# Optimization experiments

Hardware: AMD Instinct MI355X
Metric: run time of the kernel (lower is better)

The kernel has to match this reference:

```python
import jax, jax.numpy as jnp
import numpy as np

N = 100000      # num_nodes
R = 8           # num_relations
D = 128         # node feature size
EMB = 128       # embedding_size
E = 1600000     # num edges
B = 16384       # batch of triples


def setup_inputs() -> dict:
    key = jax.random.key(0)
    ks = jax.random.split(key, 10)
    edge_src = jax.random.randint(ks[0], (E,), 0, N, dtype=jnp.int32)
    edge_dst = jax.random.randint(ks[1], (E,), 0, N, dtype=jnp.int32)
    edge_rel = jax.random.randint(ks[2], (E,), 0, R, dtype=jnp.int32)
    tri_nodes = jax.random.randint(ks[3], (B, 2), 0, N, dtype=jnp.int32)
    tri_rel = jax.random.randint(ks[4], (B,), 0, R, dtype=jnp.int32)
    X = jax.random.normal(ks[5], (N, D), dtype=jnp.float32)            # frozen node features
    W_rel = jax.random.normal(ks[6], (R, D, EMB), dtype=jnp.float32) * (1.0 / np.sqrt(D))
    W_self = jax.random.normal(ks[7], (D, EMB), dtype=jnp.float32) * (1.0 / np.sqrt(D))
    b = jnp.zeros((EMB,), dtype=jnp.float32)
    rel_emb = jax.random.normal(ks[8], (R, EMB), dtype=jnp.float32) * (1.0 / np.sqrt(EMB))  # xavier-ish
    return {"X": X, "W_rel": W_rel, "W_self": W_self, "b": b, "rel_emb": rel_emb,
            "edge_src": edge_src, "edge_dst": edge_dst, "edge_rel": edge_rel,
            "tri_nodes": tri_nodes, "tri_rel": tri_rel}


def _rgcn_layer(X, W_rel, W_self, b, edge_src, edge_dst, edge_rel):
    # per-relation transformed features: [R, N, EMB]
    XW = jnp.einsum('nd,rde->rne', X, W_rel)
    # gather per-edge messages: [E, EMB]
    msg = XW[edge_rel, edge_src]
    # RGCN normalization 1/c_{i,r}: count of (dst, rel) pairs
    comb = edge_dst.astype(jnp.int32) * R + edge_rel
    cnt = jax.ops.segment_sum(jnp.ones_like(comb, dtype=jnp.float32), comb, num_segments=N * R)
    norm = 1.0 / jnp.maximum(cnt[comb], 1.0)
    agg = jax.ops.segment_sum(msg * norm[:, None], edge_dst, num_segments=N)  # [N, EMB]
    return jax.nn.relu(agg + X @ W_self + b)


def reference(X, W_rel, W_self, b, rel_emb, edge_src, edge_dst, edge_rel, tri_nodes, tri_rel):
    H = _rgcn_layer(X, W_rel, W_self, b, edge_src, edge_dst, edge_rel)  # [N, EMB]
    subj = H[tri_nodes[:, 0]]          # [B, EMB]
    obj = H[tri_nodes[:, 1]]           # [B, EMB]
    rel = rel_emb[tri_rel]             # [B, EMB]
    scores = jnp.sum(subj * rel * obj, axis=1, keepdims=True)  # [B, 1]
    return scores
```

## Files before the change

### kernel.cpp

```cpp
#include <hip/hip_runtime.h>

typedef float f32x4 __attribute__((ext_vector_type(4)));
typedef short bf16x8 __attribute__((ext_vector_type(8)));

__device__ __forceinline__ unsigned short f2bf(float f) {
  unsigned int u = __float_as_uint(f);
  u += 0x7FFFu + ((u >> 16) & 1u);
  return (unsigned short)(u >> 16);
}

__global__ void k_build_map(const int* __restrict__ tri_nodes, int* __restrict__ map,
                            int* __restrict__ uniq, int* __restrict__ counter, int n) {
  int i = blockIdx.x * blockDim.x + threadIdx.x;
  if (i >= n) return;
  int node = tri_nodes[i];
  int old = atomicCAS(&map[node], -1, -2);
  if (old == -1) {
    int mid = atomicAdd(counter, 1);
    uniq[mid] = node;
    map[node] = mid;
  }
}

__global__ void k_count(const int* __restrict__ edst, const int* __restrict__ erel,
                        const int* __restrict__ map, int* __restrict__ cnt_c, int E) {
  int stride = gridDim.x * blockDim.x;
  for (int i = blockIdx.x * blockDim.x + threadIdx.x; i < E; i += stride) {
    int mid = map[edst[i]];
    if (mid >= 0) atomicAdd(&cnt_c[mid * 8 + erel[i]], 1);
  }
}

__global__ __launch_bounds__(256) void k_scan_s1(const int* __restrict__ cnt_c,
                                                 int* __restrict__ bsum) {
  __shared__ int sh[256];
  int tid = threadIdx.x;
  int base = blockIdx.x * 1024 + tid * 4;
  int s = cnt_c[base] + cnt_c[base + 1] + cnt_c[base + 2] + cnt_c[base + 3];
  sh[tid] = s;
  __syncthreads();
  for (int o = 1; o < 256; o <<= 1) {
    int x = (tid >= o) ? sh[tid - o] : 0;
    __syncthreads();
    sh[tid] += x;
    __syncthreads();
  }
  if (tid == 255) bsum[blockIdx.x] = sh[255];
}
__global__ __launch_bounds__(256) void k_scan_s2(int* __restrict__ bsum,
                                                 int* __restrict__ seg_start, int M) {
  __shared__ int sh[256];
  int tid = threadIdx.x;
  int v = bsum[tid];
  sh[tid] = v;
  __syncthreads();
  for (int o = 1; o < 256; o <<= 1) {
    int x = (tid >= o) ? sh[tid - o] : 0;
    __syncthreads();
    sh[tid] += x;
    __syncthreads();
  }
  bsum[tid] = sh[tid] - v;
  if (tid == 255) seg_start[M] = sh[255];
}
__global__ __launch_bounds__(256) void k_scan_s3(const int* __restrict__ cnt_c,
                                                 const int* __restrict__ bsum,
                                                 int* __restrict__ seg_start,
                                                 int* __restrict__ seg_ofs) {
  __shared__ int sh[256];
  int tid = threadIdx.x;
  int base = blockIdx.x * 1024 + tid * 4;
  int c0 = cnt_c[base], c1 = cnt_c[base + 1], c2 = cnt_c[base + 2], c3 = cnt_c[base + 3];
  int s = c0 + c1 + c2 + c3;
  sh[tid] = s;
  __syncthreads();
  for (int o = 1; o < 256; o <<= 1) {
    int x = (tid >= o) ? sh[tid - o] : 0;
    __syncthreads();
    sh[tid] += x;
    __syncthreads();
  }
  int run = bsum[blockIdx.x] + sh[tid] - s;
  seg_start[base] = run; seg_ofs[base] = run; run += c0;
  seg_start[base + 1] = run; seg_ofs[base + 1] = run; run += c1;
  seg_start[base + 2] = run; seg_ofs[base + 2] = run; run += c2;
  seg_start[base + 3] = run; seg_ofs[base + 3] = run;
}

__global__ void k_scatter(const int* __restrict__ esrc, const int* __restrict__ edst,
                          const int* __restrict__ erel, const int* __restrict__ map,
                          int* __restrict__ seg_ofs, int* __restrict__ s_src, int E) {
  int stride = gridDim.x * blockDim.x;
  for (int i = blockIdx.x * blockDim.x + threadIdx.x; i < E; i += stride) {
    int mid = map[edst[i]];
    if (mid >= 0) {
      int comb = mid * 8 + erel[i];
      int pos = atomicAdd(&seg_ofs[comb], 1);
      s_src[pos] = esrc[i];
    }
  }
}

__global__ void k_cvt_w(const float* __restrict__ W_rel, const float* __restrict__ W_self,
                        unsigned short* __restrict__ Wt) {
  int i = blockIdx.x * 256 + threadIdx.x;
  if (i >= 9 * 16384) return;
  int r = i >> 14, rem = i & 16383;
  int e = rem >> 7, d = rem & 127;
  float v = (r < 8) ? W_rel[r * 16384 + d * 128 + e] : W_self[d * 128 + e];
  Wt[i] = f2bf(v);
}

__global__ __launch_bounds__(512) void k_fused(
    const float* __restrict__ X, const unsigned short* __restrict__ Wt,
    const float* __restrict__ bvec, const int* __restrict__ uniq,
    const int* __restrict__ counter, const int* __restrict__ seg_start,
    const int* __restrict__ s_src, float* __restrict__ Hacc) {
  __shared__ __align__(16) unsigned short a_lds[64 * 128];
  __shared__ __align__(16) unsigned short w_lds[128 * 128];

  int nm = *counter;
  int mid0 = blockIdx.x * 64;
  if (mid0 >= nm) return;

  int t = threadIdx.x;
  int er = t >> 3, oct = t & 7;
  int lane = t & 63, l15 = lane & 15, lg = lane >> 4;
  int wid = t >> 6, wr = wid >> 2, wc = wid & 3;
  int mid = mid0 + er;

  f32x4 acc[2][2];
#pragma unroll
  for (int m = 0; m < 2; ++m)
#pragma unroll
    for (int n = 0; n < 2; ++n) {
      f32x4 z = {0.f, 0.f, 0.f, 0.f};
      acc[m][n] = z;
    }

  for (int r = 0; r < 9; ++r) {
    __syncthreads();

    {
      const uint4* wg = (const uint4*)(Wt + r * 16384);
#pragma unroll
      for (int i = 0; i < 4; ++i) {
        int v = t + i * 512;
        int u = v ^ ((v >> 4) & 7);
        *(uint4*)&w_lds[u * 8] = wg[v];
      }
    }

    {
      float aa[16];
#pragma unroll
      for (int q = 0; q < 16; ++q) aa[q] = 0.f;
      if (r < 8) {
        int comb = mid * 8 + r;
        int s0 = seg_start[comb], s1 = seg_start[comb + 1];
        for (int e = s0; e < s1; ++e) {
          const float4* xr = (const float4*)(X + (size_t)s_src[e] * 128) + oct * 4;
#pragma unroll
          for (int q = 0; q < 4; ++q) {
            float4 v = xr[q];
            aa[q * 4 + 0] += v.x; aa[q * 4 + 1] += v.y;
            aa[q * 4 + 2] += v.z; aa[q * 4 + 3] += v.w;
          }
        }
        int cnt = s1 - s0;
        if (cnt > 1) {
          float sc = 1.0f / (float)cnt;
#pragma unroll
          for (int q = 0; q < 16; ++q) aa[q] *= sc;
        }
      } else if (mid < nm) {
        const float4* xr = (const float4*)(X + (size_t)uniq[mid] * 128) + oct * 4;
#pragma unroll
        for (int q = 0; q < 4; ++q) {
          float4 v = xr[q];
          aa[q * 4 + 0] = v.x; aa[q * 4 + 1] = v.y;
          aa[q * 4 + 2] = v.z; aa[q * 4 + 3] = v.w;
        }
      }
      unsigned int p[8];
#pragma unroll
      for (int q = 0; q < 8; ++q)
        p[q] = (unsigned int)f2bf(aa[q * 2]) | ((unsigned int)f2bf(aa[q * 2 + 1]) << 16);
      int unit0 = er * 16 + oct * 2, sw = er & 7;
      uint4 p0 = make_uint4(p[0], p[1], p[2], p[3]);
      uint4 p1 = make_uint4(p[4], p[5], p[6], p[7]);
      *(uint4*)&a_lds[((unit0) ^ sw) * 8] = p0;
      *(uint4*)&a_lds[((unit0 + 1) ^ sw) * 8] = p1;
    }
    __syncthreads();

#pragma unroll
    for (int kb = 0; kb < 4; ++kb) {
      int ku = kb * 4 + lg;
      bf16x8 af[2], bfr[2];
#pragma unroll
      for (int m = 0; m < 2; ++m) {
        int row = wr * 32 + m * 16 + l15;
        af[m] = *(const bf16x8*)&a_lds[((row * 16 + ku) ^ (row & 7)) * 8];
      }
#pragma unroll
      for (int n = 0; n < 2; ++n) {
        int col = wc * 32 + n * 16 + l15;
        bfr[n] = *(const bf16x8*)&w_lds[((col * 16 + ku) ^ (col & 7)) * 8];
      }
#pragma unroll
      for (int m = 0; m < 2; ++m)
#pragma unroll
        for (int n = 0; n < 2; ++n)
          acc[m][n] = __builtin_amdgcn_mfma_f32_16x16x32_bf16(af[m], bfr[n], acc[m][n], 0, 0, 0);
    }
  }

#pragma unroll
  for (int m = 0; m < 2; ++m) {
#pragma unroll
    for (int n = 0; n < 2; ++n) {
      int col = wc * 32 + n * 16 + l15;
      float bv = bvec[col];
#pragma unroll
      for (int q = 0; q < 4; ++q) {
        int row = mid0 + wr * 32 + m * 16 + lg * 4 + q;
        float v = acc[m][n][q] + bv;
        Hacc[(size_t)row * 128 + col] = v > 0.f ? v : 0.f;
      }
    }
  }
}

__global__ void k_score(const float* __restrict__ H, const int* __restrict__ map,
                        const float* __restrict__ rel_emb, const int* __restrict__ tri_nodes,
                        const int* __restrict__ tri_rel, float* __restrict__ out, int B) {
  int w = (blockIdx.x * blockDim.x + threadIdx.x) >> 6;
  int lane = threadIdx.x & 63;
  if (w >= B) return;
  int s = map[tri_nodes[w * 2]];
  int o = map[tri_nodes[w * 2 + 1]];
  const float* hs = H + (size_t)s * 128;
  const float* ho = H + (size_t)o * 128;
  const float* rr = rel_emb + (size_t)tri_rel[w] * 128;
  float p = hs[lane] * ho[lane] * rr[lane] + hs[lane + 64] * ho[lane + 64] * rr[lane + 64];
#pragma unroll
  for (int ofs = 32; ofs > 0; ofs >>= 1) p += __shfl_down(p, ofs);
  if (lane == 0) out[w] = p;
}

extern "C" void kernel_launch(void* const* d_in, const int* in_sizes, int n_in,
                              void* d_out, int out_size, void* d_ws, size_t ws_size,
                              hipStream_t stream) {
  const float* X       = (const float*)d_in[0];
  const float* W_rel   = (const float*)d_in[1];
  const float* W_self  = (const float*)d_in[2];
  const float* bvec    = (const float*)d_in[3];
  const float* rel_emb = (const float*)d_in[4];
  const int* edge_src  = (const int*)d_in[5];
  const int* edge_dst  = (const int*)d_in[6];
  const int* edge_rel  = (const int*)d_in[7];
  const int* tri_nodes = (const int*)d_in[8];
  const int* tri_rel   = (const int*)d_in[9];

  int N  = in_sizes[0] / 128;
  int E  = in_sizes[5];
  int nt = in_sizes[8];
  int B  = in_sizes[9];
  int M  = nt * 8;

  char* ws = (char*)d_ws;
  int* map       = (int*)ws;
  int* counter   = map + N;
  int* uniq      = counter + 64;
  int* cnt_c     = uniq + nt;
  int* seg_start = cnt_c + M;
  int* seg_ofs   = seg_start + M + 64;
  int* bsum      = seg_ofs + M;
  int* s_src     = bsum + 256;
  float* Hacc    = (float*)(s_src + E);
  unsigned short* Wt = (unsigned short*)cnt_c;

  hipMemsetAsync(map, 0xFF, (size_t)N * 4, stream);
  hipMemsetAsync(counter, 0, 64 * 4, stream);
  hipMemsetAsync(cnt_c, 0, (size_t)M * 4, stream);

  k_build_map<<<(nt + 255) / 256, 256, 0, stream>>>(tri_nodes, map, uniq, counter, nt);
  k_count<<<1024, 256, 0, stream>>>(edge_dst, edge_rel, map, cnt_c, E);
  k_scan_s1<<<256, 256, 0, stream>>>(cnt_c, bsum);
  k_scan_s2<<<1, 256, 0, stream>>>(bsum, seg_start, M);
  k_scan_s3<<<256, 256, 0, stream>>>(cnt_c, bsum, seg_start, seg_ofs);
  k_cvt_w<<<(9 * 16384 + 255) / 256, 256, 0, stream>>>(W_rel, W_self, Wt);
  k_scatter<<<1024, 256, 0, stream>>>(edge_src, edge_dst, edge_rel, map, seg_ofs,
                                      s_src, E);
  k_fused<<<nt / 64, 512, 0, stream>>>(X, Wt, bvec, uniq, counter, seg_start, s_src, Hacc);
  k_score<<<(B * 64 + 255) / 256, 256, 0, stream>>>(Hacc, map, rel_emb, tri_nodes,
                                                    tri_rel, (float*)d_out, B);
}
```

Before: 146.3 us.

## Make segments relation-major and aggregate block edges cooperatively via LDS atomics

Segments are now laid out relation-major (rel*nt + mid), so the 64 nodes of a block occupy one contiguous edge range per relation. All 512 threads stride over that range, decoding the destination row from a packed (mid<<17 | src) word and accumulating X rows into an LDS float buffer with atomics. This replaces the old scheme where each row of 8 threads walked its own segment serially. The aim is to remove load imbalance between rows and expose more memory parallelism in the gather. W fragments are now read straight from global into registers instead of being staged through LDS. The cost is extra LDS atomics, an additional barrier per relation, and hardcoded assumptions (base uses r*32768, so nt must be 32768, and src must fit in 17 bits).

```diff
diff --git a/kernel.cpp b/kernel.cpp
--- a/kernel.cpp
+++ b/kernel.cpp
@@ -23,11 +23,12 @@
 }
 
 __global__ void k_count(const int* __restrict__ edst, const int* __restrict__ erel,
-                        const int* __restrict__ map, int* __restrict__ cnt_c, int E) {
+                        const int* __restrict__ map, int* __restrict__ cnt_c,
+                        int nt, int E) {
   int stride = gridDim.x * blockDim.x;
   for (int i = blockIdx.x * blockDim.x + threadIdx.x; i < E; i += stride) {
     int mid = map[edst[i]];
-    if (mid >= 0) atomicAdd(&cnt_c[mid * 8 + erel[i]], 1);
+    if (mid >= 0) atomicAdd(&cnt_c[erel[i] * nt + mid], 1);
   }
 }
 
@@ -89,14 +90,15 @@
 
 __global__ void k_scatter(const int* __restrict__ esrc, const int* __restrict__ edst,
                           const int* __restrict__ erel, const int* __restrict__ map,
-                          int* __restrict__ seg_ofs, int* __restrict__ s_src, int E) {
+                          int* __restrict__ seg_ofs, int* __restrict__ s_pk,
+                          int nt, int E) {
   int stride = gridDim.x * blockDim.x;
   for (int i = blockIdx.x * blockDim.x + threadIdx.x; i < E; i += stride) {
     int mid = map[edst[i]];
     if (mid >= 0) {
-      int comb = mid * 8 + erel[i];
+      int comb = erel[i] * nt + mid;
       int pos = atomicAdd(&seg_ofs[comb], 1);
-      s_src[pos] = esrc[i];
+      s_pk[pos] = (mid << 17) | esrc[i];
     }
   }
 }
@@ -115,9 +117,9 @@
     const float* __restrict__ X, const unsigned short* __restrict__ Wt,
     const float* __restrict__ bvec, const int* __restrict__ uniq,
     const int* __restrict__ counter, const int* __restrict__ seg_start,
-    const int* __restrict__ s_src, float* __restrict__ Hacc) {
+    const int* __restrict__ s_pk, float* __restrict__ Hacc) {
+  __shared__ float a_acc[64 * 132];
   __shared__ __align__(16) unsigned short a_lds[64 * 128];
-  __shared__ __align__(16) unsigned short w_lds[128 * 128];
 
   int nm = *counter;
   int mid0 = blockIdx.x * 64;
@@ -127,7 +129,6 @@
   int er = t >> 3, oct = t & 7;
   int lane = t & 63, l15 = lane & 15, lg = lane >> 4;
   int wid = t >> 6, wr = wid >> 2, wc = wid & 3;
-  int mid = mid0 + er;
 
   f32x4 acc[2][2];
 #pragma unroll
@@ -141,39 +142,49 @@
   for (int r = 0; r < 9; ++r) {
     __syncthreads();
 
+    bf16x8 bfr[2][4];
     {
-      const uint4* wg = (const uint4*)(Wt + r * 16384);
-#pragma unroll
-      for (int i = 0; i < 4; ++i) {
-        int v = t + i * 512;
-        int u = v ^ ((v >> 4) & 7);
-        *(uint4*)&w_lds[u * 8] = wg[v];
+      const unsigned short* wb = Wt + r * 16384;
+#pragma unroll
+      for (int n = 0; n < 2; ++n)
+#pragma unroll
+        for (int kb = 0; kb < 4; ++kb)
+          bfr[n][kb] = *(const bf16x8*)(wb + (wc * 32 + n * 16 + l15) * 128 + (kb * 4 + lg) * 8);
+    }
+
+    float aa[16];
+    if (r < 8) {
+      for (int i = t; i < 64 * 132; i += 512) a_acc[i] = 0.f;
+      __syncthreads();
+
+      int base = r * 32768 + mid0;
+      int e0 = seg_start[base], e1 = seg_start[base + 64];
+      for (int p = t >> 3; e0 + p < e1; p += 64) {
+        unsigned pk = (unsigned)s_pk[e0 + p];
+        int src = pk & 0x1FFFF;
+        int row = (int)(pk >> 17) - mid0;
+        const float4* xr = (const float4*)(X + (size_t)src * 128) + oct * 4;
+        float* dst = a_acc + row * 132 + oct * 16;
+#pragma unroll
+        for (int q = 0; q < 4; ++q) {
+          float4 v = xr[q];
+          atomicAdd(dst + q * 4 + 0, v.x);
+          atomicAdd(dst + q * 4 + 1, v.y);
+          atomicAdd(dst + q * 4 + 2, v.z);
+          atomicAdd(dst + q * 4 + 3, v.w);
+        }
       }
-    }
-
-    {
-      float aa[16];
-#pragma unroll
-      for (int q = 0; q < 16; ++q) aa[q] = 0.f;
-      if (r < 8) {
-        int comb = mid * 8 + r;
-        int s0 = seg_start[comb], s1 = seg_start[comb + 1];
-        for (int e = s0; e < s1; ++e) {
-          const float4* xr = (const float4*)(X + (size_t)s_src[e] * 128) + oct * 4;
-#pragma unroll
-          for (int q = 0; q < 4; ++q) {
-            float4 v = xr[q];
-            aa[q * 4 + 0] += v.x; aa[q * 4 + 1] += v.y;
-            aa[q * 4 + 2] += v.z; aa[q * 4 + 3] += v.w;
-          }
-        }
-        int cnt = s1 - s0;
-        if (cnt > 1) {
-          float sc = 1.0f / (float)cnt;
-#pragma unroll
-          for (int q = 0; q < 16; ++q) aa[q] *= sc;
-        }
-      } else if (mid < nm) {
+      __syncthreads();
+
+      int cnt = seg_start[base + er + 1] - seg_start[base + er];
+      float sc = (cnt > 1) ? (1.0f / (float)cnt) : 1.0f;
+#pragma unroll
+      for (int j = 0; j < 16; ++j) aa[j] = a_acc[er * 132 + oct * 16 + j] * sc;
+    } else {
+#pragma unroll
+      for (int j = 0; j < 16; ++j) aa[j] = 0.f;
+      int mid = mid0 + er;
+      if (mid < nm) {
         const float4* xr = (const float4*)(X + (size_t)uniq[mid] * 128) + oct * 4;
 #pragma unroll
         for (int q = 0; q < 4; ++q) {
@@ -182,6 +193,9 @@
           aa[q * 4 + 2] = v.z; aa[q * 4 + 3] = v.w;
         }
       }
+    }
+
+    {
       unsigned int p[8];
 #pragma unroll
       for (int q = 0; q < 8; ++q)
@@ -197,22 +211,17 @@
 #pragma unroll
     for (int kb = 0; kb < 4; ++kb) {
       int ku = kb * 4 + lg;
-      bf16x8 af[2], bfr[2];
+      bf16x8 af[2];
 #pragma unroll
       for (int m = 0; m < 2; ++m) {
         int row = wr * 32 + m * 16 + l15;
         af[m] = *(const bf16x8*)&a_lds[((row * 16 + ku) ^ (row & 7)) * 8];
       }
 #pragma unroll
-      for (int n = 0; n < 2; ++n) {
-        int col = wc * 32 + n * 16 + l15;
-        bfr[n] = *(const bf16x8*)&w_lds[((col * 16 + ku) ^ (col & 7)) * 8];
-      }
-#pragma unroll
       for (int m = 0; m < 2; ++m)
 #pragma unroll
         for (int n = 0; n < 2; ++n)
-          acc[m][n] = __builtin_amdgcn_mfma_f32_16x16x32_bf16(af[m], bfr[n], acc[m][n], 0, 0, 0);
+          acc[m][n] = __builtin_amdgcn_mfma_f32_16x16x32_bf16(af[m], bfr[n][kb], acc[m][n], 0, 0, 0);
     }
   }
 
@@ -277,8 +286,8 @@
   int* seg_start = cnt_c + M;
   int* seg_ofs   = seg_start + M + 64;
   int* bsum      = seg_ofs + M;
-  int* s_src     = bsum + 256;
-  float* Hacc    = (float*)(s_src + E);
+  int* s_pk      = bsum + 256;
+  float* Hacc    = (float*)(s_pk + E);
   unsigned short* Wt = (unsigned short*)cnt_c;
 
   hipMemsetAsync(map, 0xFF, (size_t)N * 4, stream);
@@ -286,14 +295,14 @@
   hipMemsetAsync(cnt_c, 0, (size_t)M * 4, stream);
 
   k_build_map<<<(nt + 255) / 256, 256, 0, stream>>>(tri_nodes, map, uniq, counter, nt);
-  k_count<<<1024, 256, 0, stream>>>(edge_dst, edge_rel, map, cnt_c, E);
+  k_count<<<1024, 256, 0, stream>>>(edge_dst, edge_rel, map, cnt_c, nt, E);
   k_scan_s1<<<256, 256, 0, stream>>>(cnt_c, bsum);
   k_scan_s2<<<1, 256, 0, stream>>>(bsum, seg_start, M);
   k_scan_s3<<<256, 256, 0, stream>>>(cnt_c, bsum, seg_start, seg_ofs);
   k_cvt_w<<<(9 * 16384 + 255) / 256, 256, 0, stream>>>(W_rel, W_self, Wt);
   k_scatter<<<1024, 256, 0, stream>>>(edge_src, edge_dst, edge_rel, map, seg_ofs,
-                                      s_src, E);
-  k_fused<<<nt / 64, 512, 0, stream>>>(X, Wt, bvec, uniq, counter, seg_start, s_src, Hacc);
+                                      s_pk, nt, E);
+  k_fused<<<nt / 64, 512, 0, stream>>>(X, Wt, bvec, uniq, counter, seg_start, s_pk, Hacc);
   k_score<<<(B * 64 + 255) / 256, 256, 0, stream>>>(Hacc, map, rel_emb, tri_nodes,
                                                     tri_rel, (float*)d_out, B);
 }
```

Result: slower. 474.2 us (+224.1%).

## Shrink fused tile to 16 rows, read MFMA-fragment weights directly from global

Applied to the files above, without the earlier changes.

The fused gather+GEMM kernel now processes 16 unique nodes per 256-thread block instead of 64 per 512-thread block. This yields four times as many blocks and more parallel latency hiding for the irregular edge gathers. The weights are pre-packed into MFMA fragment order so each wave loads B fragments straight from global or L2, and the 32 KB weight staging in LDS per relation is dropped. The edge count and scatter kernels switch from grid-stride loops to one thread per edge. The cost is more redundant weight traffic per block, since each block rereads all nine weight matrices through cache.

```diff
diff --git a/kernel.cpp b/kernel.cpp
--- a/kernel.cpp
+++ b/kernel.cpp
@@ -24,11 +24,10 @@
 
 __global__ void k_count(const int* __restrict__ edst, const int* __restrict__ erel,
                         const int* __restrict__ map, int* __restrict__ cnt_c, int E) {
-  int stride = gridDim.x * blockDim.x;
-  for (int i = blockIdx.x * blockDim.x + threadIdx.x; i < E; i += stride) {
-    int mid = map[edst[i]];
-    if (mid >= 0) atomicAdd(&cnt_c[mid * 8 + erel[i]], 1);
-  }
+  int i = blockIdx.x * blockDim.x + threadIdx.x;
+  if (i >= E) return;
+  int mid = map[edst[i]];
+  if (mid >= 0) atomicAdd(&cnt_c[mid * 8 + erel[i]], 1);
 }
 
 __global__ __launch_bounds__(256) void k_scan_s1(const int* __restrict__ cnt_c,
@@ -90,144 +89,113 @@
 __global__ void k_scatter(const int* __restrict__ esrc, const int* __restrict__ edst,
                           const int* __restrict__ erel, const int* __restrict__ map,
                           int* __restrict__ seg_ofs, int* __restrict__ s_src, int E) {
-  int stride = gridDim.x * blockDim.x;
-  for (int i = blockIdx.x * blockDim.x + threadIdx.x; i < E; i += stride) {
-    int mid = map[edst[i]];
-    if (mid >= 0) {
-      int comb = mid * 8 + erel[i];
-      int pos = atomicAdd(&seg_ofs[comb], 1);
-      s_src[pos] = esrc[i];
-    }
+  int i = blockIdx.x * blockDim.x + threadIdx.x;
+  if (i >= E) return;
+  int mid = map[edst[i]];
+  if (mid >= 0) {
+    int comb = mid * 8 + erel[i];
+    int pos = atomicAdd(&seg_ofs[comb], 1);
+    s_src[pos] = esrc[i];
   }
 }
 
 __global__ void k_cvt_w(const float* __restrict__ W_rel, const float* __restrict__ W_self,
-                        unsigned short* __restrict__ Wt) {
+                        unsigned short* __restrict__ Wf) {
   int i = blockIdx.x * 256 + threadIdx.x;
   if (i >= 9 * 16384) return;
-  int r = i >> 14, rem = i & 16383;
-  int e = rem >> 7, d = rem & 127;
-  float v = (r < 8) ? W_rel[r * 16384 + d * 128 + e] : W_self[d * 128 + e];
-  Wt[i] = f2bf(v);
-}
-
-__global__ __launch_bounds__(512) void k_fused(
-    const float* __restrict__ X, const unsigned short* __restrict__ Wt,
+  int j = i & 7;
+  int tmp = i >> 3;
+  int col = tmp & 127;
+  int ku = (tmp >> 7) & 15;
+  int r = tmp >> 11;
+  int d = ku * 8 + j;
+  float v = (r < 8) ? W_rel[r * 16384 + d * 128 + col] : W_self[d * 128 + col];
+  Wf[i] = f2bf(v);
+}
+
+__global__ __launch_bounds__(256) void k_fused(
+    const float* __restrict__ X, const unsigned short* __restrict__ Wf,
     const float* __restrict__ bvec, const int* __restrict__ uniq,
     const int* __restrict__ counter, const int* __restrict__ seg_start,
     const int* __restrict__ s_src, float* __restrict__ Hacc) {
-  __shared__ __align__(16) unsigned short a_lds[64 * 128];
-  __shared__ __align__(16) unsigned short w_lds[128 * 128];
+  __shared__ __align__(16) unsigned short a_lds[16 * 128];
 
   int nm = *counter;
-  int mid0 = blockIdx.x * 64;
+  int mid0 = blockIdx.x * 16;
   if (mid0 >= nm) return;
 
   int t = threadIdx.x;
-  int er = t >> 3, oct = t & 7;
+  int er = t >> 4, seg = t & 15;
   int lane = t & 63, l15 = lane & 15, lg = lane >> 4;
-  int wid = t >> 6, wr = wid >> 2, wc = wid & 3;
+  int wc = t >> 6;
   int mid = mid0 + er;
 
-  f32x4 acc[2][2];
-#pragma unroll
-  for (int m = 0; m < 2; ++m)
-#pragma unroll
-    for (int n = 0; n < 2; ++n) {
-      f32x4 z = {0.f, 0.f, 0.f, 0.f};
-      acc[m][n] = z;
-    }
+  f32x4 acc[2];
+  {
+    f32x4 z = {0.f, 0.f, 0.f, 0.f};
+    acc[0] = z; acc[1] = z;
+  }
 
   for (int r = 0; r < 9; ++r) {
     __syncthreads();
 
     {
-      const uint4* wg = (const uint4*)(Wt + r * 16384);
-#pragma unroll
-      for (int i = 0; i < 4; ++i) {
-        int v = t + i * 512;
-        int u = v ^ ((v >> 4) & 7);
-        *(uint4*)&w_lds[u * 8] = wg[v];
-      }
-    }
-
-    {
-      float aa[16];
-#pragma unroll
-      for (int q = 0; q < 16; ++q) aa[q] = 0.f;
+      float aa[8];
+#pragma unroll
+      for (int q = 0; q < 8; ++q) aa[q] = 0.f;
       if (r < 8) {
         int comb = mid * 8 + r;
         int s0 = seg_start[comb], s1 = seg_start[comb + 1];
         for (int e = s0; e < s1; ++e) {
-          const float4* xr = (const float4*)(X + (size_t)s_src[e] * 128) + oct * 4;
-#pragma unroll
-          for (int q = 0; q < 4; ++q) {
-            float4 v = xr[q];
-            aa[q * 4 + 0] += v.x; aa[q * 4 + 1] += v.y;
-            aa[q * 4 + 2] += v.z; aa[q * 4 + 3] += v.w;
-          }
+          const float4* xr = (const float4*)(X + (size_t)s_src[e] * 128) + seg * 2;
+          float4 v0 = xr[0], v1 = xr[1];
+          aa[0] += v0.x; aa[1] += v0.y; aa[2] += v0.z; aa[3] += v0.w;
+          aa[4] += v1.x; aa[5] += v1.y; aa[6] += v1.z; aa[7] += v1.w;
         }
         int cnt = s1 - s0;
         if (cnt > 1) {
           float sc = 1.0f / (float)cnt;
 #pragma unroll
-          for (int q = 0; q < 16; ++q) aa[q] *= sc;
+          for (int q = 0; q < 8; ++q) aa[q] *= sc;
         }
       } else if (mid < nm) {
-        const float4* xr = (const float4*)(X + (size_t)uniq[mid] * 128) + oct * 4;
-#pragma unroll
-        for (int q = 0; q < 4; ++q) {
-          float4 v = xr[q];
-          aa[q * 4 + 0] = v.x; aa[q * 4 + 1] = v.y;
-          aa[q * 4 + 2] = v.z; aa[q * 4 + 3] = v.w;
-        }
+        const float4* xr = (const float4*)(X + (size_t)uniq[mid] * 128) + seg * 2;
+        float4 v0 = xr[0], v1 = xr[1];
+        aa[0] = v0.x; aa[1] = v0.y; aa[2] = v0.z; aa[3] = v0.w;
+        aa[4] = v1.x; aa[5] = v1.y; aa[6] = v1.z; aa[7] = v1.w;
       }
-      unsigned int p[8];
-#pragma unroll
-      for (int q = 0; q < 8; ++q)
-        p[q] = (unsigned int)f2bf(aa[q * 2]) | ((unsigned int)f2bf(aa[q * 2 + 1]) << 16);
-      int unit0 = er * 16 + oct * 2, sw = er & 7;
-      uint4 p0 = make_uint4(p[0], p[1], p[2], p[3]);
-      uint4 p1 = make_uint4(p[4], p[5], p[6], p[7]);
-      *(uint4*)&a_lds[((unit0) ^ sw) * 8] = p0;
-      *(uint4*)&a_lds[((unit0 + 1) ^ sw) * 8] = p1;
+      uint4 p;
+      p.x = (unsigned int)f2bf(aa[0]) | ((unsigned int)f2bf(aa[1]) << 16);
+      p.y = (unsigned int)f2bf(aa[2]) | ((unsigned int)f2bf(aa[3]) << 16);
+      p.z = (unsigned int)f2bf(aa[4]) | ((unsigned int)f2bf(aa[5]) << 16);
+      p.w = (unsigned int)f2bf(aa[6]) | ((unsigned int)f2bf(aa[7]) << 16);
+      *(uint4*)&a_lds[(((er * 16 + seg) ^ (er & 7)) * 8)] = p;
     }
     __syncthreads();
 
+    const unsigned short* wf = Wf + r * 16384;
 #pragma unroll
     for (int kb = 0; kb < 4; ++kb) {
       int ku = kb * 4 + lg;
-      bf16x8 af[2], bfr[2];
-#pragma unroll
-      for (int m = 0; m < 2; ++m) {
-        int row = wr * 32 + m * 16 + l15;
-        af[m] = *(const bf16x8*)&a_lds[((row * 16 + ku) ^ (row & 7)) * 8];
-      }
+      bf16x8 af = *(const bf16x8*)&a_lds[((l15 * 16 + ku) ^ (l15 & 7)) * 8];
 #pragma unroll
       for (int n = 0; n < 2; ++n) {
         int col = wc * 32 + n * 16 + l15;
-        bfr[n] = *(const bf16x8*)&w_lds[((col * 16 + ku) ^ (col & 7)) * 8];
+        bf16x8 bfr = *(const bf16x8*)(wf + ((size_t)(ku * 128 + col)) * 8);
+        acc[n] = __builtin_amdgcn_mfma_f32_16x16x32_bf16(af, bfr, acc[n], 0, 0, 0);
       }
-#pragma unroll
-      for (int m = 0; m < 2; ++m)
-#pragma unroll
-        for (int n = 0; n < 2; ++n)
-          acc[m][n] = __builtin_amdgcn_mfma_f32_16x16x32_bf16(af[m], bfr[n], acc[m][n], 0, 0, 0);
     }
   }
 
 #pragma unroll
-  for (int m = 0; m < 2; ++m) {
-#pragma unroll
-    for (int n = 0; n < 2; ++n) {
-      int col = wc * 32 + n * 16 + l15;
-      float bv = bvec[col];
-#pragma unroll
-      for (int q = 0; q < 4; ++q) {
-        int row = mid0 + wr * 32 + m * 16 + lg * 4 + q;
-        float v = acc[m][n][q] + bv;
-        Hacc[(size_t)row * 128 + col] = v > 0.f ? v : 0.f;
-      }
+  for (int n = 0; n < 2; ++n) {
+    int col = wc * 32 + n * 16 + l15;
+    float bv = bvec[col];
+#pragma unroll
+    for (int q = 0; q < 4; ++q) {
+      int row = mid0 + lg * 4 + q;
+      float v = acc[n][q] + bv;
+      Hacc[(size_t)row * 128 + col] = v > 0.f ? v : 0.f;
     }
   }
 }
@@ -279,21 +247,22 @@
   int* bsum      = seg_ofs + M;
   int* s_src     = bsum + 256;
   float* Hacc    = (float*)(s_src + E);
-  unsigned short* Wt = (unsigned short*)cnt_c;
+  unsigned short* Wf = (unsigned short*)cnt_c;
 
   hipMemsetAsync(map, 0xFF, (size_t)N * 4, stream);
   hipMemsetAsync(counter, 0, 64 * 4, stream);
   hipMemsetAsync(cnt_c, 0, (size_t)M * 4, stream);
 
+  int eblocks = (E + 255) / 256;
   k_build_map<<<(nt + 255) / 256, 256, 0, stream>>>(tri_nodes, map, uniq, counter, nt);
-  k_count<<<1024, 256, 0, stream>>>(edge_dst, edge_rel, map, cnt_c, E);
+  k_count<<<eblocks, 256, 0, stream>>>(edge_dst, edge_rel, map, cnt_c, E);
   k_scan_s1<<<256, 256, 0, stream>>>(cnt_c, bsum);
   k_scan_s2<<<1, 256, 0, stream>>>(bsum, seg_start, M);
   k_scan_s3<<<256, 256, 0, stream>>>(cnt_c, bsum, seg_start, seg_ofs);
-  k_cvt_w<<<(9 * 16384 + 255) / 256, 256, 0, stream>>>(W_rel, W_self, Wt);
-  k_scatter<<<1024, 256, 0, stream>>>(edge_src, edge_dst, edge_rel, map, seg_ofs,
-                                      s_src, E);
-  k_fused<<<nt / 64, 512, 0, stream>>>(X, Wt, bvec, uniq, counter, seg_start, s_src, Hacc);
+  k_cvt_w<<<(9 * 16384 + 255) / 256, 256, 0, stream>>>(W_rel, W_self, Wf);
+  k_scatter<<<eblocks, 256, 0, stream>>>(edge_src, edge_dst, edge_rel, map, seg_ofs,
+                                         s_src, E);
+  k_fused<<<nt / 16, 256, 0, stream>>>(X, Wf, bvec, uniq, counter, seg_start, s_src, Hacc);
   k_score<<<(B * 64 + 255) / 256, 256, 0, stream>>>(Hacc, map, rel_emb, tri_nodes,
                                                     tri_rel, (float*)d_out, B);
 }
```

Measured after the change: 137.7 us. 5.9% less time.
